# Performance work log

Hardware: AMD Instinct MI355X
Metric: run time of the kernel (lower is better)

Reference implementation:

```python
import jax, jax.numpy as jnp
import numpy as np

B, N, HID, NHEADS, VOCAB = 8, 2048, 768, 4, 15
ALPHA = 0.2  # LeakyReLU negative slope
NEG = -9e15  # matches -9000000000000000.0 mask constant


def setup_inputs() -> dict:
    key = jax.random.key(0)
    ks = jax.random.split(key, 7)
    node_feats = jax.random.randint(ks[0], (B, N), 0, VOCAB, dtype=jnp.int32)
    adjs = jax.random.randint(ks[1], (B, N, N), 0, 2, dtype=jnp.int32)
    embed_table = jax.random.normal(ks[2], (VOCAB, HID), dtype=jnp.float32)
    W_heads = jax.random.normal(ks[3], (NHEADS, HID, HID), dtype=jnp.float32) * 0.05
    a_heads = jax.random.normal(ks[4], (NHEADS, 2 * HID, 1), dtype=jnp.float32) * 0.05
    W_out = jax.random.normal(ks[5], (NHEADS * HID, HID), dtype=jnp.float32) * 0.05
    a_out = jax.random.normal(ks[6], (2 * HID, 1), dtype=jnp.float32) * 0.05
    return {"node_feats": node_feats, "adjs": adjs, "embed_table": embed_table,
            "W_heads": W_heads, "a_heads": a_heads, "W_out": W_out, "a_out": a_out}


def gat_layer(h, adj, W, a, concat):
    # h: (B,N,Fin), adj: (B,N,N), W: (Fin,Fout), a: (2*Fout,1)
    Fout = W.shape[1]
    Wh = jnp.matmul(h, W)                      # (B,N,Fout)
    Wh1 = jnp.matmul(Wh, a[:Fout])             # (B,N,1)
    Wh2 = jnp.matmul(Wh, a[Fout:])             # (B,N,1)
    e = Wh1 + jnp.swapaxes(Wh2, 1, 2)          # (B,N,N)
    e = jax.nn.leaky_relu(e, negative_slope=ALPHA)
    e = jnp.where(adj > 0, e, NEG)
    att = jax.nn.softmax(e, axis=-1)           # (B,N,N)
    h_prime = jnp.matmul(att, Wh)              # (B,N,Fout)
    return jax.nn.elu(h_prime) if concat else h_prime


def reference(node_feats, adjs, embed_table, W_heads, a_heads, W_out, a_out):
    x = embed_table[node_feats]                # (B,N,HID)  (shape_enc treated as identity)
    # multi-head GAT, heads vmapped then concatenated along feature dim
    heads = jax.vmap(lambda W, a: gat_layer(x, adjs, W, a, concat=True))(W_heads, a_heads)
    x = jnp.concatenate(jnp.moveaxis(heads, 0, -2).reshape(B, N, 1, NHEADS * HID).squeeze(2)[None], axis=0)[0] if False else jnp.transpose(heads, (1, 2, 0, 3)).reshape(B, N, NHEADS * HID)
    x = jax.nn.elu(gat_layer(x, adjs, W_out, a_out, concat=False))  # (B,N,HID)
    # pooling_forward with all-ones mask -> masked mean over node dim
    sum_emb = jnp.sum(x, axis=1)               # (B,HID)
    denom = jnp.maximum(jnp.full_like(sum_emb, float(N)), 1e-9)
    return sum_emb / denom                     # (B,HID)
```

## Files before the change

kernel.cpp:

```cpp
#include <hip/hip_runtime.h>
#include <math.h>

#define BB 8
#define NN 2048
#define HID 768
#define NHEADS 4
#define VOCAB 15
#define ALPHA 0.2f
#define NEGV -9e15f
#define MTOT (BB * NN)

using short4v = __attribute__((ext_vector_type(4))) short;
using short8v = __attribute__((ext_vector_type(8))) short;
using f32x4 = __attribute__((ext_vector_type(4))) float;

__device__ __forceinline__ short f2bf(float f) {
  union { float f; unsigned u; } x;
  x.f = f;
  unsigned r = x.u + 0x7fffu + ((x.u >> 16) & 1u);
  return (short)(r >> 16);
}

__device__ __forceinline__ void cp16(const void* g, void* l) {
  __builtin_amdgcn_global_load_lds(
      (const __attribute__((address_space(1))) unsigned int*)g,
      (__attribute__((address_space(3))) unsigned int*)l, 16, 0, 0);
}

__device__ __forceinline__ unsigned long long nibcompress(unsigned long long x) {
  x = (x | (x >> 4)) & 0x00FF00FF00FF00FFull;
  x = (x | (x >> 8)) & 0x0000FFFF0000FFFFull;
  x = (x | (x >> 16)) & 0x00000000FFFFFFFFull;
  return x;
}

#define PACK_B 32768
#define ZERO_B 308
#define NFM_B 64
#define TRAN_B 2304
#define TW_B 192
__global__ __launch_bounds__(256) void setup_kernel(
    const int* __restrict__ adj, unsigned long long* __restrict__ packed,
    float* __restrict__ zbase, const int* __restrict__ nf,
    unsigned long long* __restrict__ nfm, const float* __restrict__ W_out,
    short* __restrict__ Wt_o, const float* __restrict__ table,
    const float* __restrict__ W_heads, float* __restrict__ TWp) {
  const int bid = blockIdx.x;
  const int tid = threadIdx.x;
  if (bid < PACK_B) {
    __shared__ unsigned long long nibq[32];
    long base = (long)bid * 1024;
    int4 a = *(const int4*)(adj + base + tid * 4);
    unsigned nib = (a.x > 0 ? 1u : 0u) | (a.y > 0 ? 2u : 0u) |
                   (a.z > 0 ? 4u : 0u) | (a.w > 0 ? 8u : 0u);
    ((unsigned char*)nibq)[tid] = (unsigned char)nib;
    __syncthreads();
    if (tid < 16) {
      unsigned long long lo = nibcompress(nibq[2 * tid]);
      unsigned long long hi = nibcompress(nibq[2 * tid + 1]);
      packed[(base >> 6) + tid] = lo | (hi << 32);
    }
  } else if (bid < PACK_B + ZERO_B) {
    zbase[(bid - PACK_B) * 256 + tid] = 0.f;
  } else if (bid < PACK_B + ZERO_B + NFM_B) {
    int r = bid - PACK_B - ZERO_B;
    int b = r >> 3, c = r & 7;
    int w = tid >> 6;
    int j = c * 256 + tid;
    int nfv = nf[b * NN + j];
#pragma unroll
    for (int v = 0; v < VOCAB; ++v) {
      unsigned long long m = __ballot(nfv == v);
      if ((tid & 63) == 0) nfm[((long)b * VOCAB + v) * 32 + c * 4 + w] = m;
    }
  } else if (bid < PACK_B + ZERO_B + NFM_B + TRAN_B) {
    __shared__ float t[32][33];
    int r2 = bid - PACK_B - ZERO_B - NFM_B;
    const int K = NHEADS * HID, N = HID;
    int k0 = (r2 % 96) * 32, n0 = (r2 / 96) * 32;
    int tx = tid & 31, ty = tid >> 5;
#pragma unroll
    for (int i = 0; i < 32; i += 8)
      t[ty + i][tx] = W_out[(long)(k0 + ty + i) * N + n0 + tx];
    __syncthreads();
#pragma unroll
    for (int i = 0; i < 32; i += 8)
      Wt_o[(long)(n0 + ty + i) * K + k0 + tx] = f2bf(t[tx][ty + i]);
  } else {
    __shared__ float tbl[VOCAB][48];
    int r3 = bid - PACK_B - ZERO_B - NFM_B - TRAN_B;
    const int cx = r3 % 12, ky = r3 / 12;
    const int c = cx * 256 + tid;
    const int h = (cx * 256) / HID;
    const int n = c - h * HID;
    const int k0 = ky * 48;
    for (int idx = tid; idx < VOCAB * 48; idx += 256)
      tbl[idx / 48][idx % 48] = table[(idx / 48) * HID + k0 + idx % 48];
    __syncthreads();
    float acc[VOCAB];
#pragma unroll
    for (int v = 0; v < VOCAB; ++v) acc[v] = 0.f;
    const float* wp = W_heads + (long)h * HID * HID + (long)k0 * HID + n;
#pragma unroll 8
    for (int kk = 0; kk < 48; ++kk) {
      float w = wp[(long)kk * HID];
#pragma unroll
      for (int v = 0; v < VOCAB; ++v) acc[v] = fmaf(tbl[v][kk], w, acc[v]);
    }
#pragma unroll
    for (int v = 0; v < VOCAB; ++v)
      TWp[((long)ky * VOCAB + v) * (NHEADS * HID) + c] = acc[v];
  }
}

__global__ __launch_bounds__(256) void tw_finish_kernel(
    const float* __restrict__ TWp, float* __restrict__ TW,
    const float* __restrict__ a_heads, float* __restrict__ TW1,
    float* __restrict__ TW2) {
  const int tid = threadIdx.x;
  const int c = blockIdx.x * 256 + tid;
  const int h = (blockIdx.x * 256) / HID;
  const int n = c - h * HID;
  const float a1 = a_heads[h * 2 * HID + n];
  const float a2 = a_heads[h * 2 * HID + HID + n];
  const int lane = tid & 63;
  const int wv = tid >> 6;
  __shared__ float red[4][2 * VOCAB];

  float s1[VOCAB], s2[VOCAB];
#pragma unroll
  for (int v = 0; v < VOCAB; ++v) {
    float s = 0.f;
#pragma unroll
    for (int ky = 0; ky < 16; ++ky)
      s += TWp[((long)ky * VOCAB + v) * (NHEADS * HID) + c];
    TW[v * (NHEADS * HID) + c] = s;
    s1[v] = s * a1;
    s2[v] = s * a2;
  }
#pragma unroll
  for (int off = 1; off < 64; off <<= 1)
#pragma unroll
    for (int v = 0; v < VOCAB; ++v) {
      s1[v] += __shfl_xor(s1[v], off);
      s2[v] += __shfl_xor(s2[v], off);
    }
  if (lane == 0) {
#pragma unroll
    for (int v = 0; v < VOCAB; ++v) {
      red[wv][v] = s1[v];
      red[wv][VOCAB + v] = s2[v];
    }
  }
  __syncthreads();
  if (tid < 2 * VOCAB) {
    float s = red[0][tid] + red[1][tid] + red[2][tid] + red[3][tid];
    float* dst = (tid < VOCAB) ? (TW1 + h * VOCAB + tid)
                               : (TW2 + h * VOCAB + tid - VOCAB);
    atomicAdd(dst, s);
  }
}

__global__ __launch_bounds__(256) void p16_kernel(
    const int* __restrict__ nf, const unsigned* __restrict__ padj32,
    const unsigned* __restrict__ nfm32, const float* __restrict__ TW1,
    const float* __restrict__ TW2, float* __restrict__ P16) {
  const int t = threadIdx.x;
  const int wv = t >> 6;
  const int lane = t & 63;
  const int rowm = blockIdx.x * 4 + wv;
  const int b = rowm >> 11;
  __shared__ float cnts[4][16];

  unsigned a = padj32[(long)rowm * 64 + lane];
  const unsigned* nb = nfm32 + (long)b * VOCAB * 64 + lane;
  int cnt[VOCAB];
#pragma unroll
  for (int v = 0; v < VOCAB; ++v) cnt[v] = __popc(a & nb[v * 64]);
#pragma unroll
  for (int off = 1; off < 64; off <<= 1)
#pragma unroll
    for (int v = 0; v < VOCAB; ++v) cnt[v] += __shfl_xor(cnt[v], off);
  int cntsum = 0;
#pragma unroll
  for (int v = 0; v < VOCAB; ++v) cntsum += cnt[v];
  const bool use_full = (cntsum == 0);
  if (use_full) {
#pragma unroll
    for (int v = 0; v < VOCAB; ++v) cnt[v] = __popc(nb[v * 64]);
#pragma unroll
    for (int off = 1; off < 64; off <<= 1)
#pragma unroll
      for (int v = 0; v < VOCAB; ++v) cnt[v] += __shfl_xor(cnt[v], off);
  }
  if (lane < 16) cnts[wv][lane] = (lane < VOCAB) ? (float)cnt[lane] : 0.f;
  __syncthreads();

  const int h = lane >> 4;
  const int v = lane & 15;
  const int nfi = nf[b * NN + (rowm & 2047)];
  float cvf = cnts[wv][v];
  bool valid = (v < VOCAB) && (cvf > 0.f);
  float logit = 0.f;
  if (!use_full) {
    float s = TW1[h * VOCAB + nfi] + ((v < VOCAB) ? TW2[h * VOCAB + v] : 0.f);
    logit = s > 0.f ? s : ALPHA * s;
  }
  float mv = valid ? logit : -INFINITY;
#pragma unroll
  for (int off = 1; off < 16; off <<= 1) mv = fmaxf(mv, __shfl_xor(mv, off));
  float pv = valid ? cvf * __expf(logit - mv) : 0.f;
  float sum = pv;
#pragma unroll
  for (int off = 1; off < 16; off <<= 1) sum += __shfl_xor(sum, off);
  if (v < VOCAB) P16[((long)h * 16384 + rowm) * 16 + v] = pv / sum;
}

__global__ __launch_bounds__(256) void hcat_expand(
    const float* __restrict__ TW, const float* __restrict__ P16,
    short* __restrict__ hcat) {
  __shared__ float twl[VOCAB * 128];
  __shared__ float pl[128 * 16];
  const int c0 = blockIdx.x * 128;
  const int r0 = blockIdx.y * 128;
  const int h = c0 / HID;
  const int t = threadIdx.x;
  for (int idx = t; idx < VOCAB * 128; idx += 256)
    twl[idx] = TW[(idx / 128) * (NHEADS * HID) + c0 + (idx & 127)];
  for (int idx = t; idx < 128 * 16; idx += 256)
    pl[idx] = P16[((long)h * 16384 + r0 + (idx >> 4)) * 16 + (idx & 15)];
  __syncthreads();
  const int clb = (t & 31) * 4;
  const int rlb = (t >> 5) * 16;
#pragma unroll 4
  for (int rr = 0; rr < 16; ++rr) {
    int rl = rlb + rr;
    short4v o;
#pragma unroll
    for (int cc = 0; cc < 4; ++cc) {
      float s = 0.f;
#pragma unroll
      for (int vv = 0; vv < VOCAB; ++vv)
        s = fmaf(pl[rl * 16 + vv], twl[vv * 128 + clb + cc], s);
      s = s > 0.f ? s : (__expf(s) - 1.f);
      o[cc] = f2bf(s);
    }
    *(short4v*)(hcat + (long)(r0 + rl) * (NHEADS * HID) + c0 + clb) = o;
  }
}

template <int MODE>
__global__ __launch_bounds__(256, 4) void mfma_gemm(
    const short* __restrict__ A, const short* __restrict__ B,
    int K, int lda, int ldb, long sA, long sB,
    float* __restrict__ Cf, short* __restrict__ Ct,
    const float* __restrict__ a_vec, float* __restrict__ Wh1g,
    float* __restrict__ Wh2g) {
  __shared__ short smem[8704];
  short* As = smem;
  short* Bs = smem + 4096;

  const int gx = gridDim.x, gy = gridDim.y;
  int lin = blockIdx.x + gx * (blockIdx.y + gy * blockIdx.z);
  const int per = (gx * gy * gridDim.z) >> 3;
  int work = (lin & 7) * per + (lin >> 3);
  const int bx = work % gx;
  int tmp = work / gx;
  const int by = tmp % gy;
  const int z = tmp / gy;

  A += (long)z * sA;
  B += (long)z * sB;

  const int tid = threadIdx.x;
  const int m0 = by * 128;
  const int n0 = bx * 128;

  const int lane = tid & 63;
  const int wid = tid >> 6;
  const int wm = (wid & 1) * 64;
  const int wn = (wid >> 1) * 64;
  const int l15 = lane & 15;
  const int quad = lane >> 4;
  const int cp = quad ^ ((l15 >> 1) & 3);

  f32x4 acc[4][4];
#pragma unroll
  for (int i = 0; i < 4; ++i)
#pragma unroll
    for (int j = 0; j < 4; ++j) acc[i][j] = (f32x4){0.f, 0.f, 0.f, 0.f};

  for (int k0 = 0; k0 < K; k0 += 32) {
#pragma unroll
    for (int it = 0; it < 2; ++it) {
      int lin2 = it * 256 + tid;
      int r = lin2 >> 2;
      int p = lin2 & 3;
      int kc = p ^ ((r >> 1) & 3);
      cp16(A + (long)(m0 + r) * lda + k0 + kc * 8, &As[lin2 * 8]);
    }
#pragma unroll
    for (int it = 0; it < 2; ++it) {
      int lin2 = it * 256 + tid;
      int r = lin2 >> 2;
      int p = lin2 & 3;
      int kc = p ^ ((r >> 1) & 3);
      cp16(B + (long)(n0 + r) * ldb + k0 + kc * 8, &Bs[lin2 * 8]);
    }
    __syncthreads();

    short8v af[4], bfr[4];
#pragma unroll
    for (int i = 0; i < 4; ++i)
      af[i] = *(const short8v*)(As + (wm + i * 16 + l15) * 32 + cp * 8);
#pragma unroll
    for (int j = 0; j < 4; ++j)
      bfr[j] = *(const short8v*)(Bs + (wn + j * 16 + l15) * 32 + cp * 8);
#pragma unroll
    for (int i = 0; i < 4; ++i)
#pragma unroll
      for (int j = 0; j < 4; ++j)
        acc[i][j] = __builtin_amdgcn_mfma_f32_16x16x32_bf16(af[i], bfr[j],
                                                            acc[i][j], 0, 0, 0);
    __syncthreads();
  }

  if constexpr (MODE == 3) {
#pragma unroll
    for (int j = 0; j < 4; ++j) {
      int col = n0 + wn + j * 16 + l15;
      float s = 0.f;
#pragma unroll
      for (int i = 0; i < 4; ++i)
#pragma unroll
        for (int reg = 0; reg < 4; ++reg) {
          float v = acc[i][j][reg];
          s += v > 0.f ? v : (__expf(v) - 1.f);
        }
      s += __shfl_xor(s, 16);
      s += __shfl_xor(s, 32);
      if (quad == 0) atomicAdd(Cf + (long)z * HID + col, s * (1.0f / NN));
    }
  } else {
    float a1v[4], a2v[4];
#pragma unroll
    for (int j = 0; j < 4; ++j) {
      int colh = n0 + wn + j * 16 + l15;
      a1v[j] = a_vec[colh];
      a2v[j] = a_vec[HID + colh];
    }
#pragma unroll
    for (int i = 0; i < 4; ++i) {
      int rb = m0 + wm + i * 16 + quad * 4;
#pragma unroll
      for (int reg = 0; reg < 4; ++reg) {
        float s1 = 0.f, s2 = 0.f;
#pragma unroll
        for (int j = 0; j < 4; ++j) {
          s1 = fmaf(acc[i][j][reg], a1v[j], s1);
          s2 = fmaf(acc[i][j][reg], a2v[j], s2);
        }
#pragma unroll
        for (int off = 1; off < 16; off <<= 1) {
          s1 += __shfl_xor(s1, off);
          s2 += __shfl_xor(s2, off);
        }
        if (l15 == 0) {
          atomicAdd(Wh1g + rb + reg, s1);
          atomicAdd(Wh2g + rb + reg, s2);
        }
      }
    }
    const int bb = m0 >> 11;
    const int ml0 = m0 & 2047;
#pragma unroll
    for (int p = 0; p < 2; ++p) {
      if (wn == p * 64) {
#pragma unroll
        for (int j = 0; j < 4; ++j) {
          int col_l = j * 16 + l15;
#pragma unroll
          for (int i = 0; i < 4; ++i) {
            int row_l = wm + i * 16 + quad * 4;
            short4v pk;
#pragma unroll
            for (int reg = 0; reg < 4; ++reg) pk[reg] = f2bf(acc[i][j][reg]);
            *(short4v*)(smem + col_l * 136 + row_l) = pk;
          }
        }
      }
      __syncthreads();
#pragma unroll
      for (int it = 0; it < 4; ++it) {
        int idx = it * 256 + tid;
        int col_l = idx >> 4;
        int ch = idx & 15;
        short8v ld = *(const short8v*)(smem + col_l * 136 + ch * 8);
        int colh = n0 + p * 64 + col_l;
        *(short8v*)(Ct + ((long)bb * HID + colh) * NN + ml0 + ch * 8) = ld;
      }
      __syncthreads();
    }
  }
}

__global__ __launch_bounds__(256) void attn_softmax_kernel(
    const float* __restrict__ Wh1, const float* __restrict__ Wh2,
    const unsigned long long* __restrict__ packed, short* __restrict__ att,
    float* __restrict__ zA, int zn) {
  int row = blockIdx.x;
  if (row < zn) zA[row * 256 + threadIdx.x] = 0.f;
  int b = row >> 11;
  const unsigned char* bits = (const unsigned char*)(packed + (long)row * 32);
  const float* wh2b = Wh2 + b * NN;
  const int t = threadIdx.x;
  const int lane = t & 63;
  const int wv = t >> 6;

  unsigned m8 = bits[t];
  float wh1 = Wh1[row];
  float4 wa = ((const float4*)(wh2b + t * 8))[0];
  float4 wb = ((const float4*)(wh2b + t * 8))[1];
  float v[8] = {wa.x, wa.y, wa.z, wa.w, wb.x, wb.y, wb.z, wb.w};

  float lmax = -INFINITY;
#pragma unroll
  for (int k = 0; k < 8; ++k) {
    float s = wh1 + v[k];
    s = s > 0.f ? s : ALPHA * s;
    s = ((m8 >> k) & 1u) ? s : NEGV;
    v[k] = s;
    lmax = fmaxf(lmax, s);
  }

  __shared__ float redm[4], reds[4];
#pragma unroll
  for (int off = 32; off > 0; off >>= 1) lmax = fmaxf(lmax, __shfl_xor(lmax, off));
  if (lane == 0) redm[wv] = lmax;
  __syncthreads();
  float m = fmaxf(fmaxf(redm[0], redm[1]), fmaxf(redm[2], redm[3]));

  float lsum = 0.f;
#pragma unroll
  for (int k = 0; k < 8; ++k) {
    float p = __expf(v[k] - m);
    v[k] = p;
    lsum += p;
  }
#pragma unroll
  for (int off = 32; off > 0; off >>= 1) lsum += __shfl_xor(lsum, off);
  if (lane == 0) reds[wv] = lsum;
  __syncthreads();
  float inv = 1.f / (reds[0] + reds[1] + reds[2] + reds[3]);

  short8v o;
#pragma unroll
  for (int k = 0; k < 8; ++k) o[k] = f2bf(v[k] * inv);
  *(short8v*)(att + (long)row * NN + t * 8) = o;
}

extern "C" void kernel_launch(void* const* d_in, const int* in_sizes, int n_in,
                              void* d_out, int out_size, void* d_ws,
                              size_t ws_size, hipStream_t stream) {
  const int* node_feats = (const int*)d_in[0];
  const int* adjs = (const int*)d_in[1];
  const float* embed_table = (const float*)d_in[2];
  const float* W_heads = (const float*)d_in[3];
  const float* a_heads = (const float*)d_in[4];
  const float* W_out = (const float*)d_in[5];
  const float* a_out = (const float*)d_in[6];
  float* out = (float*)d_out;

  char* p = (char*)d_ws;
  short* Wt_o = (short*)p;  p += (size_t)HID * (NHEADS * HID) * 2;
  short* Wh_t = (short*)p;  p += (size_t)BB * HID * NN * 2;
  short* att2 = (short*)p;  p += (size_t)BB * NN * NN * 2;
  short* hcat = (short*)p;  p += (size_t)MTOT * NHEADS * HID * 2;
  unsigned long long* padj = (unsigned long long*)p;
  p += (size_t)BB * NN * NN / 8;
  float* P16 = (float*)p;   p += (size_t)NHEADS * 16384 * 16 * 4;
  float* Wh1 = (float*)p;   p += (size_t)16384 * 4;
  float* Wh2 = (float*)p;   p += (size_t)16384 * 4;
  float* TW1 = (float*)p;   p += (size_t)64 * 4;
  float* TW2 = (float*)p;   p += (size_t)64 * 4;
  p += (size_t)(ZERO_B * 256 - 2 * 16384 - 128) * 4;
  float* TWp = (float*)p;   p += (size_t)16 * VOCAB * NHEADS * HID * 4;
  float* TW = (float*)p;    p += (size_t)VOCAB * NHEADS * HID * 4;
  unsigned long long* nfm = (unsigned long long*)p;
  p += (size_t)BB * VOCAB * 32 * 8;
  if ((size_t)(p - (char*)d_ws) > ws_size) return;

  setup_kernel<<<PACK_B + ZERO_B + NFM_B + TRAN_B + TW_B, 256, 0, stream>>>(
      adjs, padj, Wh1, node_feats, nfm, W_out, Wt_o, embed_table, W_heads,
      TWp);

  tw_finish_kernel<<<12, 256, 0, stream>>>(TWp, TW, a_heads, TW1, TW2);
  p16_kernel<<<16384 / 4, 256, 0, stream>>>(
      node_feats, (const unsigned*)padj, (const unsigned*)nfm, TW1, TW2, P16);
  hcat_expand<<<dim3(24, 128), 256, 0, stream>>>(TW, P16, hcat);

  mfma_gemm<0><<<dim3(HID / 128, MTOT / 128, 1), 256, 0, stream>>>(
      hcat, Wt_o, NHEADS * HID, NHEADS * HID, NHEADS * HID, 0, 0,
      nullptr, Wh_t, a_out, Wh1, Wh2);
  attn_softmax_kernel<<<MTOT, 256, 0, stream>>>(Wh1, Wh2, padj, att2, out, 24);
  mfma_gemm<3><<<dim3(HID / 128, NN / 128, BB), 256, 0, stream>>>(
      att2, Wh_t, NN, NN, NN, (long)NN * NN, (long)HID * NN,
      out, nullptr, nullptr, nullptr, nullptr);
}
```

Baseline: 440.2 us.

## Rewrite MFMA GEMM as 256x256 tile with double-buffered async LDS pipeline

After: 439.8 us. Within noise of the previous version (-0.1%).

```diff
diff --git a/kernel.cpp b/kernel.cpp
--- a/kernel.cpp
+++ b/kernel.cpp
@@ -33,6 +33,14 @@
   x = (x | (x >> 16)) & 0x00000000FFFFFFFFull;
   return x;
 }
+
+#define MEMFENCE asm volatile("" ::: "memory")
+#define SBAR()                         \
+  do {                                 \
+    MEMFENCE;                          \
+    __builtin_amdgcn_s_barrier();      \
+    MEMFENCE;                          \
+  } while (0)
 
 #define PACK_B 32768
 #define ZERO_B 308
@@ -250,91 +258,188 @@
 }
 
 template <int MODE>
-__global__ __launch_bounds__(256, 4) void mfma_gemm(
+__global__ __launch_bounds__(512, 2) void mfma_gemm(
     const short* __restrict__ A, const short* __restrict__ B,
     int K, int lda, int ldb, long sA, long sB,
     float* __restrict__ Cf, short* __restrict__ Ct,
     const float* __restrict__ a_vec, float* __restrict__ Wh1g,
     float* __restrict__ Wh2g) {
-  __shared__ short smem[8704];
-  short* As = smem;
-  short* Bs = smem + 4096;
+  __shared__ short lds[2][2][16384];
 
   const int gx = gridDim.x, gy = gridDim.y;
-  int lin = blockIdx.x + gx * (blockIdx.y + gy * blockIdx.z);
+  int linb = blockIdx.x + gx * (blockIdx.y + gy * blockIdx.z);
   const int per = (gx * gy * gridDim.z) >> 3;
-  int work = (lin & 7) * per + (lin >> 3);
+  int work = (linb & 7) * per + (linb >> 3);
   const int bx = work % gx;
-  int tmp = work / gx;
-  const int by = tmp % gy;
-  const int z = tmp / gy;
+  int tmpw = work / gx;
+  const int by = tmpw % gy;
+  const int z = tmpw / gy;
 
   A += (long)z * sA;
   B += (long)z * sB;
 
   const int tid = threadIdx.x;
-  const int m0 = by * 128;
-  const int n0 = bx * 128;
-
+  const int m0 = by * 256;
+  const int n0 = bx * 256;
   const int lane = tid & 63;
   const int wid = tid >> 6;
-  const int wm = (wid & 1) * 64;
-  const int wn = (wid >> 1) * 64;
+  const int wr = wid >> 2;
+  const int wc = wid & 3;
   const int l15 = lane & 15;
   const int quad = lane >> 4;
-  const int cp = quad ^ ((l15 >> 1) & 3);
-
-  f32x4 acc[4][4];
-#pragma unroll
-  for (int i = 0; i < 4; ++i)
+  const int NT = K >> 6;
+
+  const int cbase = (quad ^ (l15 & 7)) << 3;
+
+  auto stageA = [&](int kt, int h) {
+    const short* src = A + (long)(m0 + h * 128) * lda + kt * 64;
+    short* dst = &lds[kt & 1][0][h * 8192];
+#pragma unroll
+    for (int it = 0; it < 2; ++it) {
+      int r = it * 64 + (tid >> 3);
+      int s = tid & 7;
+      cp16(src + (long)r * lda + ((s ^ (r & 7)) << 3),
+           dst + (it * 512 + tid) * 8);
+    }
+  };
+  auto stageB = [&](int kt, int h) {
+    const short* src = B + (long)(n0 + h * 128) * ldb + kt * 64;
+    short* dst = &lds[kt & 1][1][h * 8192];
+#pragma unroll
+    for (int it = 0; it < 2; ++it) {
+      int r = it * 64 + (tid >> 3);
+      int s = tid & 7;
+      cp16(src + (long)r * ldb + ((s ^ (r & 7)) << 3),
+           dst + (it * 512 + tid) * 8);
+    }
+  };
+
+  f32x4 acc[8][4];
+#pragma unroll
+  for (int i = 0; i < 8; ++i)
 #pragma unroll
     for (int j = 0; j < 4; ++j) acc[i][j] = (f32x4){0.f, 0.f, 0.f, 0.f};
 
-  for (int k0 = 0; k0 < K; k0 += 32) {
-#pragma unroll
-    for (int it = 0; it < 2; ++it) {
-      int lin2 = it * 256 + tid;
-      int r = lin2 >> 2;
-      int p = lin2 & 3;
-      int kc = p ^ ((r >> 1) & 3);
-      cp16(A + (long)(m0 + r) * lda + k0 + kc * 8, &As[lin2 * 8]);
-    }
-#pragma unroll
-    for (int it = 0; it < 2; ++it) {
-      int lin2 = it * 256 + tid;
-      int r = lin2 >> 2;
-      int p = lin2 & 3;
-      int kc = p ^ ((r >> 1) & 3);
-      cp16(B + (long)(n0 + r) * ldb + k0 + kc * 8, &Bs[lin2 * 8]);
-    }
-    __syncthreads();
-
-    short8v af[4], bfr[4];
-#pragma unroll
-    for (int i = 0; i < 4; ++i)
-      af[i] = *(const short8v*)(As + (wm + i * 16 + l15) * 32 + cp * 8);
-#pragma unroll
-    for (int j = 0; j < 4; ++j)
-      bfr[j] = *(const short8v*)(Bs + (wn + j * 16 + l15) * 32 + cp * 8);
-#pragma unroll
-    for (int i = 0; i < 4; ++i)
-#pragma unroll
-      for (int j = 0; j < 4; ++j)
-        acc[i][j] = __builtin_amdgcn_mfma_f32_16x16x32_bf16(af[i], bfr[j],
-                                                            acc[i][j], 0, 0, 0);
-    __syncthreads();
+  stageA(0, 0); stageA(0, 1);
+  stageB(0, 0); stageB(0, 1);
+  stageA(1, 0); stageA(1, 1);
+  asm volatile("s_waitcnt vmcnt(4)" ::: "memory");
+  SBAR();
+
+#pragma unroll 1
+  for (int t = 0; t < NT; ++t) {
+    const int p = t & 1;
+    const short* Ab = &lds[p][0][0];
+    const short* Bb = &lds[p][1][0];
+    short8v a[4][2], b0[2][2], b1[2][2];
+
+    if (t + 1 < NT) { stageB(t + 1, 0); stageB(t + 1, 1); }
+#pragma unroll
+    for (int ii = 0; ii < 4; ++ii) {
+      int ro = (wr * 128 + ii * 16 + l15) * 64;
+      a[ii][0] = *(const short8v*)(Ab + ro + cbase);
+      a[ii][1] = *(const short8v*)(Ab + ro + (cbase ^ 32));
+    }
+#pragma unroll
+    for (int jj = 0; jj < 2; ++jj) {
+      int ro = (wc * 64 + jj * 16 + l15) * 64;
+      b0[jj][0] = *(const short8v*)(Bb + ro + cbase);
+      b0[jj][1] = *(const short8v*)(Bb + ro + (cbase ^ 32));
+    }
+    SBAR();
+    asm volatile("s_waitcnt lgkmcnt(0)" ::: "memory");
+    __builtin_amdgcn_sched_barrier(0);
+    __builtin_amdgcn_s_setprio(1);
+#pragma unroll
+    for (int ii = 0; ii < 4; ++ii)
+#pragma unroll
+      for (int jj = 0; jj < 2; ++jj) {
+        acc[ii][jj] = __builtin_amdgcn_mfma_f32_16x16x32_bf16(
+            a[ii][0], b0[jj][0], acc[ii][jj], 0, 0, 0);
+        acc[ii][jj] = __builtin_amdgcn_mfma_f32_16x16x32_bf16(
+            a[ii][1], b0[jj][1], acc[ii][jj], 0, 0, 0);
+      }
+    __builtin_amdgcn_sched_barrier(0);
+    __builtin_amdgcn_s_setprio(0);
+    SBAR();
+
+#pragma unroll
+    for (int jj = 0; jj < 2; ++jj) {
+      int ro = (wc * 64 + 32 + jj * 16 + l15) * 64;
+      b1[jj][0] = *(const short8v*)(Bb + ro + cbase);
+      b1[jj][1] = *(const short8v*)(Bb + ro + (cbase ^ 32));
+    }
+    SBAR();
+    asm volatile("s_waitcnt lgkmcnt(0)" ::: "memory");
+    __builtin_amdgcn_sched_barrier(0);
+    __builtin_amdgcn_s_setprio(1);
+#pragma unroll
+    for (int ii = 0; ii < 4; ++ii)
+#pragma unroll
+      for (int jj = 0; jj < 2; ++jj) {
+        acc[ii][2 + jj] = __builtin_amdgcn_mfma_f32_16x16x32_bf16(
+            a[ii][0], b1[jj][0], acc[ii][2 + jj], 0, 0, 0);
+        acc[ii][2 + jj] = __builtin_amdgcn_mfma_f32_16x16x32_bf16(
+            a[ii][1], b1[jj][1], acc[ii][2 + jj], 0, 0, 0);
+      }
+    __builtin_amdgcn_sched_barrier(0);
+    __builtin_amdgcn_s_setprio(0);
+    SBAR();
+
+#pragma unroll
+    for (int ii = 0; ii < 4; ++ii) {
+      int ro = (wr * 128 + 64 + ii * 16 + l15) * 64;
+      a[ii][0] = *(const short8v*)(Ab + ro + cbase);
+      a[ii][1] = *(const short8v*)(Ab + ro + (cbase ^ 32));
+    }
+    SBAR();
+    asm volatile("s_waitcnt lgkmcnt(0)" ::: "memory");
+    __builtin_amdgcn_sched_barrier(0);
+    __builtin_amdgcn_s_setprio(1);
+#pragma unroll
+    for (int ii = 0; ii < 4; ++ii)
+#pragma unroll
+      for (int jj = 0; jj < 2; ++jj) {
+        acc[4 + ii][2 + jj] = __builtin_amdgcn_mfma_f32_16x16x32_bf16(
+            a[ii][0], b1[jj][0], acc[4 + ii][2 + jj], 0, 0, 0);
+        acc[4 + ii][2 + jj] = __builtin_amdgcn_mfma_f32_16x16x32_bf16(
+            a[ii][1], b1[jj][1], acc[4 + ii][2 + jj], 0, 0, 0);
+      }
+    __builtin_amdgcn_sched_barrier(0);
+    __builtin_amdgcn_s_setprio(0);
+    SBAR();
+
+    if (t + 2 < NT) { stageA(t + 2, 0); stageA(t + 2, 1); }
+    __builtin_amdgcn_s_setprio(1);
+#pragma unroll
+    for (int ii = 0; ii < 4; ++ii)
+#pragma unroll
+      for (int jj = 0; jj < 2; ++jj) {
+        acc[4 + ii][jj] = __builtin_amdgcn_mfma_f32_16x16x32_bf16(
+            a[ii][0], b0[jj][0], acc[4 + ii][jj], 0, 0, 0);
+        acc[4 + ii][jj] = __builtin_amdgcn_mfma_f32_16x16x32_bf16(
+            a[ii][1], b0[jj][1], acc[4 + ii][jj], 0, 0, 0);
+      }
+    __builtin_amdgcn_sched_barrier(0);
+    __builtin_amdgcn_s_setprio(0);
+    if (t + 2 < NT) {
+      asm volatile("s_waitcnt vmcnt(4)" ::: "memory");
+    } else if (t + 1 < NT) {
+      asm volatile("s_waitcnt vmcnt(0)" ::: "memory");
+    }
+    SBAR();
   }
 
   if constexpr (MODE == 3) {
 #pragma unroll
-    for (int j = 0; j < 4; ++j) {
-      int col = n0 + wn + j * 16 + l15;
+    for (int nj = 0; nj < 4; ++nj) {
+      int col = n0 + wc * 64 + nj * 16 + l15;
       float s = 0.f;
 #pragma unroll
-      for (int i = 0; i < 4; ++i)
+      for (int mi = 0; mi < 8; ++mi)
 #pragma unroll
         for (int reg = 0; reg < 4; ++reg) {
-          float v = acc[i][j][reg];
+          float v = acc[mi][nj][reg];
           s += v > 0.f ? v : (__expf(v) - 1.f);
         }
       s += __shfl_xor(s, 16);
@@ -344,21 +449,21 @@
   } else {
     float a1v[4], a2v[4];
 #pragma unroll
-    for (int j = 0; j < 4; ++j) {
-      int colh = n0 + wn + j * 16 + l15;
-      a1v[j] = a_vec[colh];
-      a2v[j] = a_vec[HID + colh];
-    }
-#pragma unroll
-    for (int i = 0; i < 4; ++i) {
-      int rb = m0 + wm + i * 16 + quad * 4;
+    for (int nj = 0; nj < 4; ++nj) {
+      int colh = n0 + wc * 64 + nj * 16 + l15;
+      a1v[nj] = a_vec[colh];
+      a2v[nj] = a_vec[HID + colh];
+    }
+#pragma unroll
+    for (int mi = 0; mi < 8; ++mi) {
+      int rb = m0 + wr * 128 + mi * 16 + quad * 4;
 #pragma unroll
       for (int reg = 0; reg < 4; ++reg) {
         float s1 = 0.f, s2 = 0.f;
 #pragma unroll
-        for (int j = 0; j < 4; ++j) {
-          s1 = fmaf(acc[i][j][reg], a1v[j], s1);
-          s2 = fmaf(acc[i][j][reg], a2v[j], s2);
+        for (int nj = 0; nj < 4; ++nj) {
+          s1 = fmaf(acc[mi][nj][reg], a1v[nj], s1);
+          s2 = fmaf(acc[mi][nj][reg], a2v[nj], s2);
         }
 #pragma unroll
         for (int off = 1; off < 16; off <<= 1) {
@@ -372,34 +477,18 @@
       }
     }
     const int bb = m0 >> 11;
-    const int ml0 = m0 & 2047;
-#pragma unroll
-    for (int p = 0; p < 2; ++p) {
-      if (wn == p * 64) {
-#pragma unroll
-        for (int j = 0; j < 4; ++j) {
-          int col_l = j * 16 + l15;
-#pragma unroll
-          for (int i = 0; i < 4; ++i) {
-            int row_l = wm + i * 16 + quad * 4;
-            short4v pk;
-#pragma unroll
-            for (int reg = 0; reg < 4; ++reg) pk[reg] = f2bf(acc[i][j][reg]);
-            *(short4v*)(smem + col_l * 136 + row_l) = pk;
-          }
-        }
+    const int ml0 = (m0 & 2047) + wr * 128;
+#pragma unroll
+    for (int mi = 0; mi < 8; ++mi) {
+#pragma unroll
+      for (int nj = 0; nj < 4; ++nj) {
+        int colh = n0 + wc * 64 + nj * 16 + l15;
+        short4v pk;
+#pragma unroll
+        for (int reg = 0; reg < 4; ++reg) pk[reg] = f2bf(acc[mi][nj][reg]);
+        *(short4v*)(Ct + ((long)bb * HID + colh) * NN + ml0 + mi * 16 +
+                    quad * 4) = pk;
       }
-      __syncthreads();
-#pragma unroll
-      for (int it = 0; it < 4; ++it) {
-        int idx = it * 256 + tid;
-        int col_l = idx >> 4;
-        int ch = idx & 15;
-        short8v ld = *(const short8v*)(smem + col_l * 136 + ch * 8);
-        int colh = n0 + p * 64 + col_l;
-        *(short8v*)(Ct + ((long)bb * HID + colh) * NN + ml0 + ch * 8) = ld;
-      }
-      __syncthreads();
     }
   }
 }
@@ -499,11 +588,11 @@
       node_feats, (const unsigned*)padj, (const unsigned*)nfm, TW1, TW2, P16);
   hcat_expand<<<dim3(24, 128), 256, 0, stream>>>(TW, P16, hcat);
 
-  mfma_gemm<0><<<dim3(HID / 128, MTOT / 128, 1), 256, 0, stream>>>(
+  mfma_gemm<0><<<dim3(HID / 256, MTOT / 256, 1), 512, 0, stream>>>(
       hcat, Wt_o, NHEADS * HID, NHEADS * HID, NHEADS * HID, 0, 0,
       nullptr, Wh_t, a_out, Wh1, Wh2);
   attn_softmax_kernel<<<MTOT, 256, 0, stream>>>(Wh1, Wh2, padj, att2, out, 24);
-  mfma_gemm<3><<<dim3(HID / 128, NN / 128, BB), 256, 0, stream>>>(
+  mfma_gemm<3><<<dim3(HID / 256, NN / 256, BB), 512, 0, stream>>>(
       att2, Wh_t, NN, NN, NN, (long)NN * NN, (long)HID * NN,
       out, nullptr, nullptr, nullptr, nullptr);
 }
```
